# Optimization experiments

Hardware: AMD Instinct MI355X
Metric: run time of the kernel (lower is better)

Reference implementation:

```python
import jax, jax.numpy as jnp
import numpy as np
from jax.experimental.ode import odeint

RN = 10000   # number of radial grid points (para['rn'])
RM = 200.0   # max radius (para['rm'])
NE = 1000    # number of eigenvalue samples (evl_tr)


def setup_inputs() -> dict:
    # Match the source driver exactly: evl = linspace(-0.05, 1, 1000),
    # r_dsc = linspace(rm/rn, rm, rn).
    evl = jnp.linspace(-0.05, 1.0, NE, dtype=jnp.float32)
    r_dsc = jnp.linspace(RM / RN, RM, RN, dtype=jnp.float32)
    return {"evl": evl, "r_dsc": r_dsc}


def reference(evl, r_dsc):
    E = evl.shape[0]
    # init state: rad = 0, rad' = 1  -> shape [E, 2]
    y0 = jnp.stack([jnp.zeros((E,), evl.dtype), jnp.ones((E,), evl.dtype)], axis=-1)

    def ode_func(y, t, evl):
        rad = y[:, 0]
        rad_d = y[:, 1]
        # ptl_rs = -2/r (Coulomb potential term), broadcast over eigenvalues
        rad_dd = (-2.0 / t - evl) * rad
        return jnp.stack([rad_d, rad_dd], axis=-1)

    # dopri5 adaptive RK45, same tolerances as torchdiffeq call.
    # Output: [RN, E, 2] solution sampled at every r_dsc point.
    return odeint(ode_func, y0, r_dsc, evl, rtol=1e-6, atol=1e-9)
```

## Files before the change

### kernel.cpp

```cpp
#include <hip/hip_runtime.h>

#define NE_    1000
#define RN_    10000
#define NI_    (RN_ - 1)
#define CH_    10
#define NCH_   1000
#define SLOTS_ 64
#define CPS_   16
#define CPB_   8

__device__ __forceinline__ float rcpf(float x) { return __builtin_amdgcn_rcpf(x); }

__device__ __forceinline__ void substeps_for(int p, int& S, float& invS) {
    if (p < 16)      { S = 4; invS = 0.25f; }
    else if (p < 64) { S = 2; invS = 0.5f;  }
    else             { S = 1; invS = 1.0f;  }
}

template <int NV>
__device__ __forceinline__ void rk4_step(float q1, float q2, float q3,
                                         float h2, float h, float h6,
                                         float a[NV], float b[NV]) {
#pragma unroll
    for (int v = 0; v < NV; ++v) {
        const float ya = a[v], yb = b[v];
        const float k1a = yb;                const float k1b = q1 * ya;
        const float y2a = fmaf(h2, k1a, ya); const float y2b = fmaf(h2, k1b, yb);
        const float k2a = y2b;               const float k2b = q2 * y2a;
        const float y3a = fmaf(h2, k2a, ya); const float y3b = fmaf(h2, k2b, yb);
        const float k3a = y3b;               const float k3b = q2 * y3a;
        const float y4a = fmaf(h,  k3a, ya); const float y4b = fmaf(h,  k3b, yb);
        const float k4a = y4b;               const float k4b = q3 * y4a;
        a[v] = fmaf(h6, fmaf(2.0f, k2a + k3a, k1a + k4a), ya);
        b[v] = fmaf(h6, fmaf(2.0f, k2b + k3b, k1b + k4b), yb);
    }
}

template <int NV>
__device__ __forceinline__ void advance_interval(float ta, float tb, float e,
                                                 int S, float invS,
                                                 float a[NV], float b[NV]) {
    const float hs = (tb - ta) * invS;
    const float h2 = 0.5f * hs;
    const float h6 = hs * (1.0f / 6.0f);
    for (int j = 0; j < S; ++j) {
        const float t0 = ta + hs * (float)j;
        const float q1 = fmaf(-2.0f, rcpf(t0),      -e);
        const float q2 = fmaf(-2.0f, rcpf(t0 + h2), -e);
        const float q3 = fmaf(-2.0f, rcpf(t0 + hs), -e);
        rk4_step<NV>(q1, q2, q3, h2, hs, h6, a, b);
    }
}

__device__ __forceinline__ float4 mmul(float4 B, float4 A) {
    float4 r;
    r.x = fmaf(B.x, A.x, B.z * A.y);
    r.y = fmaf(B.y, A.x, B.w * A.y);
    r.z = fmaf(B.x, A.z, B.z * A.w);
    r.w = fmaf(B.y, A.z, B.w * A.w);
    return r;
}

__global__ __launch_bounds__(CPB_ * SLOTS_) void
k_scanfused(const float* __restrict__ evl, const float* __restrict__ t,
            float2* __restrict__ Yst) {
    __shared__ float4 lm[CPB_][SLOTS_];
    __shared__ float2 ly[CPB_][SLOTS_];

    const int tid  = threadIdx.x;
    const int eil  = tid & (CPB_ - 1);
    const int slot = tid >> 3;
    const int ei   = blockIdx.x * CPB_ + eil;

    const float e    = evl[ei];
    const float t0g  = t[0];
    const float step = (t[RN_ - 1] - t0g) * (1.0f / (float)NI_);

    float4 Mc[CPS_];
#pragma unroll
    for (int i = 0; i < CPS_; ++i) {
        const int c  = slot * CPS_ + i;
        const int p0 = c * CH_;
        const int p1 = min(p0 + CH_, NI_);
        float a2[2] = {1.0f, 0.0f};
        float b2[2] = {0.0f, 1.0f};
        if (p0 < NI_) {
            if (p0 >= 64 && p1 == p0 + CH_) {
                float tcur = fmaf((float)p0, step, t0g);
                float qcur = fmaf(-2.0f, rcpf(tcur), -e);
#pragma unroll
                for (int k = 0; k < CH_ / 2; ++k) {
                    const float pf    = (float)(p0 + 2 * k);
                    const float tmid  = fmaf(pf + 1.0f, step, t0g);
                    const float tnext = fmaf(pf + 2.0f, step, t0g);
                    const float h  = tnext - tcur;
                    const float h2 = 0.5f * h;
                    const float h6 = h * (1.0f / 6.0f);
                    const float qmid  = fmaf(-2.0f, rcpf(tmid),  -e);
                    const float qnext = fmaf(-2.0f, rcpf(tnext), -e);
                    rk4_step<2>(qcur, qmid, qnext, h2, h, h6, a2, b2);
                    tcur = tnext; qcur = qnext;
                }
            } else {
                for (int p = p0; p < p1; ++p) {
                    const float ta = fmaf((float)p,       step, t0g);
                    const float tb = fmaf((float)(p + 1), step, t0g);
                    int S; float invS; substeps_for(p, S, invS);
                    advance_interval<2>(ta, tb, e, S, invS, a2, b2);
                }
            }
        }
        Mc[i] = make_float4(a2[0], b2[0], a2[1], b2[1]);
    }

    float4 C = Mc[0];
#pragma unroll
    for (int i = 1; i < CPS_; ++i) C = mmul(Mc[i], C);
    lm[eil][slot] = C;
    __syncthreads();

    if (slot == 0) {
        float ya = 0.0f, yb = 1.0f;
#pragma unroll 8
        for (int k = 0; k < SLOTS_; ++k) {
            ly[eil][k] = make_float2(ya, yb);
            const float4 m = lm[eil][k];
            const float na = fmaf(m.x, ya, m.z * yb);
            const float nb = fmaf(m.y, ya, m.w * yb);
            ya = na; yb = nb;
        }
    }
    __syncthreads();

    const float2 y0 = ly[eil][slot];
    float ya = y0.x, yb = y0.y;
#pragma unroll
    for (int i = 0; i < CPS_; ++i) {
        const int c = slot * CPS_ + i;
        if (c < NCH_)
            Yst[(size_t)c * NE_ + ei] = make_float2(ya, yb);
        const float4 m = Mc[i];
        const float na = fmaf(m.x, ya, m.z * yb);
        const float nb = fmaf(m.y, ya, m.w * yb);
        ya = na; yb = nb;
    }
}

__global__ void k_out(const float* __restrict__ evl, const float* __restrict__ t,
                      const float2* __restrict__ Yst, float2* __restrict__ out) {
    const int tid = blockIdx.x * blockDim.x + threadIdx.x;
    if (tid >= NE_ * NCH_) return;
    const int ei = tid % NE_;
    const int c  = tid / NE_;
    const float e    = evl[ei];
    const float t0g  = t[0];
    const float step = (t[RN_ - 1] - t0g) * (1.0f / (float)NI_);
    const int p0 = c * CH_;
    const int p1 = min(p0 + CH_, NI_);
    const float2 y0 = Yst[tid];
    float a[1] = {y0.x};
    float b[1] = {y0.y};
    if (c == 0) out[ei] = make_float2(0.0f, 1.0f);
    if (p0 >= 64 && p0 + CH_ == p1) {
        float tcur = fmaf((float)p0, step, t0g);
        float qcur = fmaf(-2.0f, rcpf(tcur), -e);
#pragma unroll
        for (int k = 0; k < CH_; ++k) {
            const float pf    = (float)(p0 + k);
            const float tmid  = fmaf(pf + 0.5f, step, t0g);
            const float tnext = fmaf(pf + 1.0f, step, t0g);
            const float h  = tnext - tcur;
            const float h2 = 0.5f * h;
            const float h6 = h * (1.0f / 6.0f);
            const float qmid  = fmaf(-2.0f, rcpf(tmid),  -e);
            const float qnext = fmaf(-2.0f, rcpf(tnext), -e);
            rk4_step<1>(qcur, qmid, qnext, h2, h, h6, a, b);
            out[(size_t)(p0 + k + 1) * NE_ + ei] = make_float2(a[0], b[0]);
            tcur = tnext; qcur = qnext;
        }
    } else {
        for (int p = p0; p < p1; ++p) {
            const float ta = fmaf((float)p,       step, t0g);
            const float tb = fmaf((float)(p + 1), step, t0g);
            int S; float invS; substeps_for(p, S, invS);
            advance_interval<1>(ta, tb, e, S, invS, a, b);
            out[(size_t)(p + 1) * NE_ + ei] = make_float2(a[0], b[0]);
        }
    }
}

__global__ void k_serial(const float* __restrict__ evl, const float* __restrict__ t,
                         float2* __restrict__ out) {
    const int ei = blockIdx.x * blockDim.x + threadIdx.x;
    if (ei >= NE_) return;
    const float e    = evl[ei];
    const float t0g  = t[0];
    const float step = (t[RN_ - 1] - t0g) * (1.0f / (float)NI_);
    float a[1] = {0.0f};
    float b[1] = {1.0f};
    out[ei] = make_float2(0.0f, 1.0f);
    for (int p = 0; p < NI_; ++p) {
        const float ta = fmaf((float)p,       step, t0g);
        const float tb = fmaf((float)(p + 1), step, t0g);
        int S; float invS; substeps_for(p, S, invS);
        advance_interval<1>(ta, tb, e, S, invS, a, b);
        out[(size_t)(p + 1) * NE_ + ei] = make_float2(a[0], b[0]);
    }
}

extern "C" void kernel_launch(void* const* d_in, const int* in_sizes, int n_in,
                              void* d_out, int out_size, void* d_ws, size_t ws_size,
                              hipStream_t stream) {
    const float* evl = (const float*)d_in[0];
    const float* t   = (const float*)d_in[1];
    float2* out = (float2*)d_out;

    const size_t needYst = (size_t)NCH_ * NE_ * sizeof(float2);
    if (ws_size < needYst) {
        k_serial<<<(NE_ + 255) / 256, 256, 0, stream>>>(evl, t, out);
        return;
    }
    float2* Yst = (float2*)d_ws;

    k_scanfused<<<NE_ / CPB_, CPB_ * SLOTS_, 0, stream>>>(evl, t, Yst);
    const int ntask = NE_ * NCH_;
    k_out<<<(ntask + 255) / 256, 256, 0, stream>>>(evl, t, Yst, out);
}
```

Baseline: 124.5 us.

## Replace per-chunk transfer matrices with long segments and re-integrate chunk starts

The scan kernel now gives each thread one long segment of 160 intervals instead of 16 ten-interval chunks. It builds one 2x2 transfer matrix per segment and drops the per-chunk matrix products. After a serial block-level prefix over 64 segments, each thread re-integrates its segment with a single vector to write the chunk start states, rather than applying stored chunk matrices. This cuts register pressure and matrix-multiply work, but adds a second integration pass, a longer serial dependency chain per thread, and fewer eigenvalues per block (4 instead of 8).

```diff
diff --git a/kernel.cpp b/kernel.cpp
--- a/kernel.cpp
+++ b/kernel.cpp
@@ -5,9 +5,9 @@
 #define NI_    (RN_ - 1)
 #define CH_    10
 #define NCH_   1000
-#define SLOTS_ 64
-#define CPS_   16
-#define CPB_   8
+#define TPC_   64
+#define LSEG_  160
+#define CPB_   4
 
 __device__ __forceinline__ float rcpf(float x) { return __builtin_amdgcn_rcpf(x); }
 
@@ -52,98 +52,98 @@
     }
 }
 
-__device__ __forceinline__ float4 mmul(float4 B, float4 A) {
-    float4 r;
-    r.x = fmaf(B.x, A.x, B.z * A.y);
-    r.y = fmaf(B.y, A.x, B.w * A.y);
-    r.z = fmaf(B.x, A.z, B.z * A.w);
-    r.w = fmaf(B.y, A.z, B.w * A.w);
-    return r;
-}
-
-__global__ __launch_bounds__(CPB_ * SLOTS_) void
+template <int NV>
+__device__ __forceinline__ void advance_range(int p0, int p1, float step,
+                                              float t0g, float e,
+                                              float a[NV], float b[NV],
+                                              float2* __restrict__ YST, int ei) {
+    int p = p0;
+    while (p < p1 && p < 64) {
+        if (YST && p % CH_ == 0)
+            YST[(size_t)(p / CH_) * NE_ + ei] = make_float2(a[0], b[0]);
+        const float ta = fmaf((float)p,       step, t0g);
+        const float tb = fmaf((float)(p + 1), step, t0g);
+        int S; float invS; substeps_for(p, S, invS);
+        advance_interval<NV>(ta, tb, e, S, invS, a, b);
+        ++p;
+    }
+    if (p < p1) {
+        float tcur = fmaf((float)p, step, t0g);
+        float qcur = fmaf(-2.0f, rcpf(tcur), -e);
+        while (p + 2 <= p1) {
+            if (YST && p % CH_ == 0)
+                YST[(size_t)(p / CH_) * NE_ + ei] = make_float2(a[0], b[0]);
+            const float tmid  = fmaf((float)(p + 1), step, t0g);
+            const float tnext = fmaf((float)(p + 2), step, t0g);
+            const float h  = tnext - tcur;
+            const float h2 = 0.5f * h;
+            const float h6 = h * (1.0f / 6.0f);
+            const float qmid  = fmaf(-2.0f, rcpf(tmid),  -e);
+            const float qnext = fmaf(-2.0f, rcpf(tnext), -e);
+            rk4_step<NV>(qcur, qmid, qnext, h2, h, h6, a, b);
+            tcur = tnext; qcur = qnext; p += 2;
+        }
+        if (p < p1) {
+            if (YST && p % CH_ == 0)
+                YST[(size_t)(p / CH_) * NE_ + ei] = make_float2(a[0], b[0]);
+            const float tmid  = fmaf((float)p + 0.5f, step, t0g);
+            const float tnext = fmaf((float)(p + 1),  step, t0g);
+            const float h  = tnext - tcur;
+            const float h2 = 0.5f * h;
+            const float h6 = h * (1.0f / 6.0f);
+            const float qmid  = fmaf(-2.0f, rcpf(tmid),  -e);
+            const float qnext = fmaf(-2.0f, rcpf(tnext), -e);
+            rk4_step<NV>(qcur, qmid, qnext, h2, h, h6, a, b);
+        }
+    }
+}
+
+__global__ __launch_bounds__(CPB_ * TPC_) void
 k_scanfused(const float* __restrict__ evl, const float* __restrict__ t,
             float2* __restrict__ Yst) {
-    __shared__ float4 lm[CPB_][SLOTS_];
-    __shared__ float2 ly[CPB_][SLOTS_];
-
-    const int tid  = threadIdx.x;
-    const int eil  = tid & (CPB_ - 1);
-    const int slot = tid >> 3;
-    const int ei   = blockIdx.x * CPB_ + eil;
+    __shared__ float4 lm[CPB_][TPC_];
+    __shared__ float2 ly[CPB_][TPC_];
+
+    const int tid = threadIdx.x;
+    const int eil = tid & (CPB_ - 1);
+    const int j   = tid / CPB_;
+    const int ei  = blockIdx.x * CPB_ + eil;
 
     const float e    = evl[ei];
     const float t0g  = t[0];
     const float step = (t[RN_ - 1] - t0g) * (1.0f / (float)NI_);
-
-    float4 Mc[CPS_];
-#pragma unroll
-    for (int i = 0; i < CPS_; ++i) {
-        const int c  = slot * CPS_ + i;
-        const int p0 = c * CH_;
-        const int p1 = min(p0 + CH_, NI_);
-        float a2[2] = {1.0f, 0.0f};
-        float b2[2] = {0.0f, 1.0f};
-        if (p0 < NI_) {
-            if (p0 >= 64 && p1 == p0 + CH_) {
-                float tcur = fmaf((float)p0, step, t0g);
-                float qcur = fmaf(-2.0f, rcpf(tcur), -e);
-#pragma unroll
-                for (int k = 0; k < CH_ / 2; ++k) {
-                    const float pf    = (float)(p0 + 2 * k);
-                    const float tmid  = fmaf(pf + 1.0f, step, t0g);
-                    const float tnext = fmaf(pf + 2.0f, step, t0g);
-                    const float h  = tnext - tcur;
-                    const float h2 = 0.5f * h;
-                    const float h6 = h * (1.0f / 6.0f);
-                    const float qmid  = fmaf(-2.0f, rcpf(tmid),  -e);
-                    const float qnext = fmaf(-2.0f, rcpf(tnext), -e);
-                    rk4_step<2>(qcur, qmid, qnext, h2, h, h6, a2, b2);
-                    tcur = tnext; qcur = qnext;
-                }
-            } else {
-                for (int p = p0; p < p1; ++p) {
-                    const float ta = fmaf((float)p,       step, t0g);
-                    const float tb = fmaf((float)(p + 1), step, t0g);
-                    int S; float invS; substeps_for(p, S, invS);
-                    advance_interval<2>(ta, tb, e, S, invS, a2, b2);
-                }
+    const int p0 = j * LSEG_;
+    const int p1 = min(p0 + LSEG_, NI_);
+
+    float a2[2] = {1.0f, 0.0f};
+    float b2[2] = {0.0f, 1.0f};
+    if (p0 < p1)
+        advance_range<2>(p0, p1, step, t0g, e, a2, b2, nullptr, ei);
+    lm[eil][j] = make_float4(a2[0], b2[0], a2[1], b2[1]);
+    __syncthreads();
+
+    if (j == 0) {
+        float ya = 0.0f, yb = 1.0f;
+        for (int c0 = 0; c0 < TPC_; c0 += 8) {
+            float4 mm[8];
+#pragma unroll
+            for (int k = 0; k < 8; ++k) mm[k] = lm[eil][c0 + k];
+#pragma unroll
+            for (int k = 0; k < 8; ++k) {
+                ly[eil][c0 + k] = make_float2(ya, yb);
+                const float na = fmaf(mm[k].x, ya, mm[k].z * yb);
+                const float nb = fmaf(mm[k].y, ya, mm[k].w * yb);
+                ya = na; yb = nb;
             }
         }
-        Mc[i] = make_float4(a2[0], b2[0], a2[1], b2[1]);
-    }
-
-    float4 C = Mc[0];
-#pragma unroll
-    for (int i = 1; i < CPS_; ++i) C = mmul(Mc[i], C);
-    lm[eil][slot] = C;
+    }
     __syncthreads();
 
-    if (slot == 0) {
-        float ya = 0.0f, yb = 1.0f;
-#pragma unroll 8
-        for (int k = 0; k < SLOTS_; ++k) {
-            ly[eil][k] = make_float2(ya, yb);
-            const float4 m = lm[eil][k];
-            const float na = fmaf(m.x, ya, m.z * yb);
-            const float nb = fmaf(m.y, ya, m.w * yb);
-            ya = na; yb = nb;
-        }
-    }
-    __syncthreads();
-
-    const float2 y0 = ly[eil][slot];
-    float ya = y0.x, yb = y0.y;
-#pragma unroll
-    for (int i = 0; i < CPS_; ++i) {
-        const int c = slot * CPS_ + i;
-        if (c < NCH_)
-            Yst[(size_t)c * NE_ + ei] = make_float2(ya, yb);
-        const float4 m = Mc[i];
-        const float na = fmaf(m.x, ya, m.z * yb);
-        const float nb = fmaf(m.y, ya, m.w * yb);
-        ya = na; yb = nb;
-    }
+    const float2 y0 = ly[eil][j];
+    float a1[1] = {y0.x};
+    float b1[1] = {y0.y};
+    if (p0 < p1)
+        advance_range<1>(p0, p1, step, t0g, e, a1, b1, Yst, ei);
 }
 
 __global__ void k_out(const float* __restrict__ evl, const float* __restrict__ t,
@@ -222,7 +222,7 @@
     }
     float2* Yst = (float2*)d_ws;
 
-    k_scanfused<<<NE_ / CPB_, CPB_ * SLOTS_, 0, stream>>>(evl, t, Yst);
+    k_scanfused<<<NE_ / CPB_, CPB_ * TPC_, 0, stream>>>(evl, t, Yst);
     const int ntask = NE_ * NCH_;
     k_out<<<(ntask + 255) / 256, 256, 0, stream>>>(evl, t, Yst, out);
 }
```

New measurement: 158.9 us. +27.6%, slower.
